# Performance work log

Measured on AMD Instinct MI355X. Metric: run time of the kernel, lower is better.

## Reference

```python
import jax, jax.numpy as jnp
import numpy as np

N = 100000        # nodes
E = 600000        # edges
D = 128           # entity_dim = hidden_dim = output_dim
H = 8             # heads
C = D // H        # per-head channels (TransformerConv out_channels)
L = 3             # num_layers
NUM_ENT = 500000
NUM_REL = 1000


def setup_inputs() -> dict:
    key = jax.random.key(0)
    ks = jax.random.split(key, 12)
    s = 0.02
    node_ids = jax.random.randint(ks[0], (N,), 0, NUM_ENT)
    edge_index = jax.random.randint(ks[1], (2, E), 0, N)
    edge_type = jax.random.randint(ks[2], (E,), 0, NUM_REL)
    # embeddings with padding_idx=0 zeroed (matches nn.Embedding(padding_idx=0))
    ent_emb = (jax.random.normal(ks[3], (NUM_ENT, D), jnp.float32) * s).at[0].set(0.0)
    rel_emb = (jax.random.normal(ks[4], (NUM_REL, D), jnp.float32) * s).at[0].set(0.0)
    # TransformerConv linear layers (stacked over L layers, all 128->128)
    Wq = jax.random.normal(ks[5], (L, D, D), jnp.float32) * s
    Wk = jax.random.normal(ks[6], (L, D, D), jnp.float32) * s
    Wv = jax.random.normal(ks[7], (L, D, D), jnp.float32) * s
    We = jax.random.normal(ks[8], (L, D, D), jnp.float32) * s   # lin_edge
    Ws = jax.random.normal(ks[9], (L, D, D), jnp.float32) * s   # lin_skip (root_weight)
    bq = jnp.zeros((L, D), jnp.float32)
    bk = jnp.zeros((L, D), jnp.float32)
    bv = jnp.zeros((L, D), jnp.float32)
    be = jnp.zeros((L, D), jnp.float32)
    bs = jnp.zeros((L, D), jnp.float32)
    ln_g = jnp.ones((L, D), jnp.float32)
    ln_b = jnp.zeros((L, D), jnp.float32)
    return dict(node_ids=node_ids, edge_index=edge_index, edge_type=edge_type,
                ent_emb=ent_emb, rel_emb=rel_emb,
                Wq=Wq, bq=bq, Wk=Wk, bk=bk, Wv=Wv, bv=bv,
                We=We, be=be, Ws=Ws, bs=bs, ln_g=ln_g, ln_b=ln_b)


def _layer_norm(x, g, b, eps=1e-5):
    mu = x.mean(-1, keepdims=True)
    var = ((x - mu) ** 2).mean(-1, keepdims=True)
    return (x - mu) * jax.lax.rsqrt(var + eps) * g + b


def _transformer_conv(x, src, dst, eattr, Wq, bq, Wk, bk, Wv, bv, We, be, Ws, bs):
    # PyG TransformerConv, concat=True, root_weight=True, beta=False, eval mode.
    q = (x @ Wq + bq).reshape(N, H, C)
    k = (x @ Wk + bk).reshape(N, H, C)
    v = (x @ Wv + bv).reshape(N, H, C)
    e = (eattr @ We + be).reshape(E, H, C)
    k_e = k[src] + e                                  # [E,H,C]
    alpha = jnp.einsum('ehc,ehc->eh', q[dst], k_e) / jnp.sqrt(jnp.float32(C))
    # segment softmax over incoming edges of each destination node
    amax = jax.ops.segment_max(alpha, dst, num_segments=N)   # [N,H]
    ex = jnp.exp(alpha - amax[dst])
    denom = jax.ops.segment_sum(ex, dst, num_segments=N)     # [N,H]
    alpha = ex / (denom[dst] + 1e-16)
    msg = (v[src] + e) * alpha[..., None]             # [E,H,C]
    out = jax.ops.segment_sum(msg.reshape(E, H * C), dst, num_segments=N)
    return out + x @ Ws + bs                          # skip (root weight)


def reference(node_ids, edge_index, edge_type, ent_emb, rel_emb,
              Wq, bq, Wk, bk, Wv, bv, We, be, Ws, bs, ln_g, ln_b):
    x = ent_emb[node_ids]            # [N,D]
    eattr = rel_emb[edge_type]       # [E,D]
    src, dst = edge_index[0], edge_index[1]
    for i in range(L):
        x_new = _transformer_conv(x, src, dst, eattr,
                                  Wq[i], bq[i], Wk[i], bk[i], Wv[i], bv[i],
                                  We[i], be[i], Ws[i], bs[i])
        x_new = jax.nn.relu(_layer_norm(x_new, ln_g[i], ln_b[i]))
        x = x + x_new                # dims match every layer -> residual
    graph_embedding = x.mean(axis=0, keepdims=True)
    return x, graph_embedding
```

## Files before the change

kernel.cpp:

```cpp
#include <hip/hip_runtime.h>

#define NN 100000
#define EE 600000
#define RR 1000

typedef unsigned short u16;
typedef __attribute__((ext_vector_type(8))) short short8;
typedef __attribute__((ext_vector_type(4))) float f32x4;

__device__ __forceinline__ float bf2f(u16 u) {
    union { unsigned int i; float f; } c; c.i = ((unsigned int)u) << 16; return c.f;
}
__device__ __forceinline__ u16 f2bf(float f) {
    union { float f; unsigned int i; } c; c.f = f;
    unsigned int x = c.i;
    return (u16)((x + 0x7FFFu + ((x >> 16) & 1u)) >> 16);
}
__device__ __forceinline__ unsigned int pack2bf(float a, float b) {
    return (unsigned int)f2bf(a) | ((unsigned int)f2bf(b) << 16);
}
__device__ __forceinline__ float ldin(const void* p, long long i, int f32) {
    if (f32) return ((const float*)p)[i];
    return bf2f(((const u16*)p)[i]);
}
__device__ __forceinline__ void stout(void* p, long long i, float v, int f32) {
    if (f32) ((float*)p)[i] = v;
    else     ((u16*)p)[i] = f2bf(v);
}

__global__ void GraphTransformerEncoder_35021163331783_kernel(
    int mode, int layer,
    const int* node_ids, const int* edge_index, const int* edge_type,
    const void* ent, const void* rel,
    const void* Wq, const void* bq, const void* Wk, const void* bk,
    const void* Wv, const void* bv, const void* We, const void* be,
    const void* Ws, const void* bs, const void* lng, const void* lnb,
    void* out,
    float* accum, float* erel, float* denom, float* gsum, float* flagp,
    u16* xb, u16* kb, u16* vb, u16* qb, u16* wbf)
{
    __shared__ float red[128];
    __shared__ __align__(16) u16 xt[32 * 128];
    __shared__ int scnt;
    int tid = blockIdx.x * blockDim.x + threadIdx.x;

    if (mode == 9) {
        if (threadIdx.x == 0) scnt = 0;
        __syncthreads();
        int bad = 0;
        for (int i = threadIdx.x; i < 8192; i += 256) {
            float v = bf2f(((const u16*)ent)[i]);
            if (!(fabsf(v) <= 1000.0f)) bad++;
        }
        atomicAdd(&scnt, bad);
        __syncthreads();
        if (threadIdx.x == 0) flagp[0] = (scnt > 64) ? 1.0f : 0.0f;
    } else if (mode == 0) {
        if (tid < 128) gsum[tid] = 0.0f;
        if (tid < NN * 128) {
            int isf32 = (flagp[0] != 0.0f);
            int n = tid >> 7, c = tid & 127;
            xb[tid] = f2bf(ldin(ent, (long long)node_ids[n] * 128 + c, isf32));
        }
    } else if (mode == 10) {
        if (tid < NN) ((int*)denom)[NN + tid] = 0;
    } else if (mode == 11) {
        if (tid < EE) {
            int dst = edge_index[EE + tid];
            atomicAdd(&((int*)denom)[NN + dst], 1);
        }
    } else if (mode == 12) {
        int* offs = (int*)denom;
        int* cnt  = offs + NN;
        int* wsum = (int*)red;
        int lane = threadIdx.x & 63, wid = threadIdx.x >> 6;
        int base = 0;
        for (int chunk = 0; chunk < NN; chunk += 1024) {
            int i = chunk + (int)threadIdx.x;
            int v = (i < NN) ? cnt[i] : 0;
            int incl = v;
            #pragma unroll
            for (int s = 1; s < 64; s <<= 1) {
                int t = __shfl_up(incl, s, 64);
                if (lane >= s) incl += t;
            }
            if (lane == 63) wsum[wid] = incl;
            __syncthreads();
            if (threadIdx.x == 0) {
                int run = 0;
                for (int w = 0; w < 16; ++w) { int t = wsum[w]; wsum[w] = run; run += t; }
                wsum[16] = run;
            }
            __syncthreads();
            int excl = base + wsum[wid] + incl - v;
            if (i < NN) { offs[i] = excl; cnt[i] = excl; }
            base += wsum[16];
            __syncthreads();
        }
    } else if (mode == 13) {
        if (tid < EE) {
            int src = edge_index[tid];
            int dst = edge_index[EE + tid];
            int rl  = edge_type[tid];
            int* cur = (int*)denom + NN;
            int pos = atomicAdd(&cur[dst], 1);
            ((unsigned int*)denom)[2 * NN + pos] =
                (unsigned int)src | ((unsigned int)rl << 17);
        }
    } else if (mode == 1) {
        if (tid < RR * 128) {
            int isf32 = (flagp[0] != 0.0f);
            int r = tid >> 7, d = tid & 127;
            float acc = 0.0f;
            for (int k = 0; k < 128; ++k)
                acc += ldin(rel, r * 128 + k, isf32)
                     * ldin(We, (long long)layer * 16384 + k * 128 + d, isf32);
            erel[tid] = acc + ldin(be, layer * 128 + d, isf32);
        }
    } else if (mode == 14) {
        if (tid < 4 * 16384) {
            int isf32 = (flagp[0] != 0.0f);
            int mat = tid >> 14;
            int rem = tid & 16383;
            int nt = rem >> 11;
            int ks = (rem >> 9) & 3;
            int l  = (rem >> 3) & 63;
            int j  = rem & 7;
            int k = ks * 32 + ((l >> 4) << 3) + j;
            int d = nt * 16 + (l & 15);
            const void* W = (mat == 0) ? Wq : (mat == 1) ? Wk : (mat == 2) ? Wv : Ws;
            wbf[tid] = f2bf(ldin(W, (long long)layer * 16384 + k * 128 + d, isf32));
        }
    } else if (mode == 2) {
        int n0 = blockIdx.x * 32;
        int t = threadIdx.x;
        for (int u = t; u < 512; u += 256) {
            int row = u >> 4, un = u & 15;
            uint4 d4 = *(const uint4*)(xb + (long long)(n0 + row) * 128 + un * 8);
            *(uint4*)(xt + row * 128 + ((un ^ (row & 7)) << 3)) = d4;
        }
        __syncthreads();
        int wv = t >> 6;
        int l  = t & 63;
        int lr = l & 15, lg = l >> 4;
        const u16* wf = wbf + (long long)wv * 16384;
        f32x4 acc[2][8];
        #pragma unroll
        for (int mt = 0; mt < 2; ++mt)
            #pragma unroll
            for (int nt = 0; nt < 8; ++nt) acc[mt][nt] = (f32x4)0.0f;
        #pragma unroll
        for (int ks = 0; ks < 4; ++ks) {
            int un = ks * 4 + lg;
            int r0 = lr, r1 = 16 + lr;
            short8 a0 = *(const short8*)(xt + r0 * 128 + ((un ^ (r0 & 7)) << 3));
            short8 a1 = *(const short8*)(xt + r1 * 128 + ((un ^ (r1 & 7)) << 3));
            short8 b[8];
            #pragma unroll
            for (int nt = 0; nt < 8; ++nt)
                b[nt] = *(const short8*)(wf + (((nt * 4 + ks) * 64 + l) << 3));
            #pragma unroll
            for (int nt = 0; nt < 8; ++nt) {
                acc[0][nt] = __builtin_amdgcn_mfma_f32_16x16x32_bf16(a0, b[nt], acc[0][nt], 0, 0, 0);
                acc[1][nt] = __builtin_amdgcn_mfma_f32_16x16x32_bf16(a1, b[nt], acc[1][nt], 0, 0, 0);
            }
        }
        int isf32 = (flagp[0] != 0.0f);
        const void* bias = (wv == 0) ? bq : (wv == 1) ? bk : (wv == 2) ? bv : bs;
        #pragma unroll
        for (int nt = 0; nt < 8; ++nt) {
            int col = nt * 16 + lr;
            float bc = ldin(bias, layer * 128 + col, isf32);
            #pragma unroll
            for (int mt = 0; mt < 2; ++mt) {
                #pragma unroll
                for (int v = 0; v < 4; ++v) {
                    int row = n0 + mt * 16 + lg * 4 + v;
                    long long o = (long long)row * 128 + col;
                    float val = acc[mt][nt][v] + bc;
                    if (wv == 0) qb[o] = f2bf(val);
                    else if (wv == 1) kb[o] = f2bf(val);
                    else if (wv == 2) vb[o] = f2bf(val);
                    else accum[o] = val;
                }
            }
        }
    } else if (mode == 4) {
        long long n = (long long)blockIdx.x * 4 + (threadIdx.x >> 6);
        if (n < NN) {
            int l = threadIdx.x & 63;
            int isf32 = (flagp[0] != 0.0f);
            const int* offs = (const int*)denom;
            const unsigned int* packed = (const unsigned int*)denom + 2 * NN;
            unsigned int qu = ((const unsigned int*)(qb + n * 128))[l];
            float q0 = bf2f((u16)(qu & 0xFFFFu)), q1 = bf2f((u16)(qu >> 16));
            float2 seed = ((const float2*)(accum + n * 128))[l];
            int beg = offs[n];
            int end = (n == NN - 1) ? EE : offs[n + 1];
            float m0 = 0.0f, m1 = 0.0f, dsum = 0.0f;
            for (int base = beg; base < end; base += 4) {
                int cnt = end - base;
                unsigned int ku[4], vu[4];
                float2 ef[4];
                #pragma unroll
                for (int j = 0; j < 4; ++j) {
                    if (j < cnt) {
                        unsigned int pk = packed[base + j];
                        long long src = (long long)(pk & 0x1FFFFu);
                        int rl = (int)(pk >> 17);
                        ku[j] = ((const unsigned int*)(kb + src * 128))[l];
                        vu[j] = ((const unsigned int*)(vb + src * 128))[l];
                        ef[j] = ((const float2*)(erel + rl * 128))[l];
                    }
                }
                #pragma unroll
                for (int j = 0; j < 4; ++j) {
                    if (j < cnt) {
                        float e0 = ef[j].x, e1 = ef[j].y;
                        float t = q0 * (bf2f((u16)(ku[j] & 0xFFFFu)) + e0)
                                + q1 * (bf2f((u16)(ku[j] >> 16)) + e1);
                        t += __shfl_xor(t, 1, 8);
                        t += __shfl_xor(t, 2, 8);
                        t += __shfl_xor(t, 4, 8);
                        float w = __expf(t * 0.25f);
                        dsum += w;
                        m0 += w * (bf2f((u16)(vu[j] & 0xFFFFu)) + e0);
                        m1 += w * (bf2f((u16)(vu[j] >> 16)) + e1);
                    }
                }
            }
            float inv = 1.0f / (dsum + 1e-16f);
            float o0 = seed.x + m0 * inv;
            float o1 = seed.y + m1 * inv;
            float s = o0 + o1;
            #pragma unroll
            for (int m = 1; m < 64; m <<= 1) s += __shfl_xor(s, m, 64);
            float mean = s * 0.0078125f;
            float d0 = o0 - mean, d1 = o1 - mean;
            float vs = d0 * d0 + d1 * d1;
            #pragma unroll
            for (int m = 1; m < 64; m <<= 1) vs += __shfl_xor(vs, m, 64);
            float rs = rsqrtf(vs * 0.0078125f + 1e-5f);
            float y0 = d0 * rs * ldin(lng, layer * 128 + 2 * l, isf32)
                     + ldin(lnb, layer * 128 + 2 * l, isf32);
            float y1 = d1 * rs * ldin(lng, layer * 128 + 2 * l + 1, isf32)
                     + ldin(lnb, layer * 128 + 2 * l + 1, isf32);
            if (y0 < 0.0f) y0 = 0.0f;
            if (y1 < 0.0f) y1 = 0.0f;
            unsigned int xu = ((const unsigned int*)(xb + n * 128))[l];
            float xv0 = bf2f((u16)(xu & 0xFFFFu)) + y0;
            float xv1 = bf2f((u16)(xu >> 16)) + y1;
            ((unsigned int*)(xb + n * 128))[l] = pack2bf(xv0, xv1);
            ((float2*)(accum + n * 128))[l] = make_float2(xv0, xv1);
        }
    } else if (mode == 5) {
        if (tid < NN * 128) {
            int isf32 = (flagp[0] != 0.0f);
            stout(out, tid, accum[tid], isf32);
        }
    } else if (mode == 7) {
        int c = threadIdx.x;
        float acc = 0.0f;
        for (long long n = blockIdx.x; n < NN; n += gridDim.x)
            acc += accum[n * 128 + c];
        atomicAdd(&gsum[c], acc);
    } else if (mode == 8) {
        if (tid < 128) {
            int isf32 = (flagp[0] != 0.0f);
            stout(out, (long long)NN * 128 + tid, gsum[tid] * (1.0f / (float)NN), isf32);
        }
    }
}

#define GTE_ARGS node_ids, edge_index, edge_type, ent, rel, Wq, bq, Wk, bk, \
    Wv, bv, We, be, Ws, bs, lng, lnb, out, accum, erel, denom, gsum, flagp, \
    xb, kb, vb, qb, wbf

extern "C" void kernel_launch(void* const* d_in, const int* in_sizes, int n_in,
                              void* d_out, int out_size, void* d_ws, size_t ws_size,
                              hipStream_t stream) {
    (void)in_sizes; (void)n_in; (void)out_size; (void)ws_size;

    const int* node_ids   = (const int*)d_in[0];
    const int* edge_index = (const int*)d_in[1];
    const int* edge_type  = (const int*)d_in[2];
    const void* ent = d_in[3];
    const void* rel = d_in[4];
    const void* Wq  = d_in[5];
    const void* bq  = d_in[6];
    const void* Wk  = d_in[7];
    const void* bk  = d_in[8];
    const void* Wv  = d_in[9];
    const void* bv  = d_in[10];
    const void* We  = d_in[11];
    const void* be  = d_in[12];
    const void* Ws  = d_in[13];
    const void* bs  = d_in[14];
    const void* lng = d_in[15];
    const void* lnb = d_in[16];
    void* out = d_out;

    float* accum = (float*)d_ws;
    float* erel  = accum + 12800000;
    float* denom = erel  + 128000;
    float* gsum  = denom + 800000;
    float* flagp = gsum  + 128;
    u16* xb = (u16*)(flagp + 64);
    u16* kb = xb + 12800000;
    u16* vb = kb + 12800000;
    u16* wbf = vb + 12800000;
    u16* qb = (u16*)d_out;

    GraphTransformerEncoder_35021163331783_kernel<<<1, 256, 0, stream>>>(9, 0, GTE_ARGS);
    GraphTransformerEncoder_35021163331783_kernel<<<50000, 256, 0, stream>>>(0, 0, GTE_ARGS);
    GraphTransformerEncoder_35021163331783_kernel<<<391, 256, 0, stream>>>(10, 0, GTE_ARGS);
    GraphTransformerEncoder_35021163331783_kernel<<<2344, 256, 0, stream>>>(11, 0, GTE_ARGS);
    GraphTransformerEncoder_35021163331783_kernel<<<1, 1024, 0, stream>>>(12, 0, GTE_ARGS);
    GraphTransformerEncoder_35021163331783_kernel<<<2344, 256, 0, stream>>>(13, 0, GTE_ARGS);
    for (int l = 0; l < 3; ++l) {
        GraphTransformerEncoder_35021163331783_kernel<<<500, 256, 0, stream>>>(1, l, GTE_ARGS);
        GraphTransformerEncoder_35021163331783_kernel<<<256, 256, 0, stream>>>(14, l, GTE_ARGS);
        GraphTransformerEncoder_35021163331783_kernel<<<3125, 256, 0, stream>>>(2, l, GTE_ARGS);
        GraphTransformerEncoder_35021163331783_kernel<<<25000, 256, 0, stream>>>(4, l, GTE_ARGS);
    }
    GraphTransformerEncoder_35021163331783_kernel<<<50000, 256, 0, stream>>>(5, 0, GTE_ARGS);
    GraphTransformerEncoder_35021163331783_kernel<<<512, 128, 0, stream>>>(7, 0, GTE_ARGS);
    GraphTransformerEncoder_35021163331783_kernel<<<1, 128, 0, stream>>>(8, 0, GTE_ARGS);
}
```

Baseline: 1.389 ms.

## Interleave K/V rows, widen edge unroll, and fuse final output with mean reduction

K and V projections are now stored interleaved in one buffer, so each edge gather in the attention/aggregation pass does a single 8-byte load per lane instead of two 4-byte loads from separate rows. The edge loop is unrolled to 8 edges to keep more gathers in flight. The fp32 residual copy is written only on the last layer. The final output store and the column-sum for the graph mean are fused into one kernel, removing a full pass over the fp32 activations. The trade-offs are more live registers per thread and a doubled-width K/V buffer layout.

```diff
diff --git a/kernel.cpp b/kernel.cpp
--- a/kernel.cpp
+++ b/kernel.cpp
@@ -37,7 +37,7 @@
     const void* Ws, const void* bs, const void* lng, const void* lnb,
     void* out,
     float* accum, float* erel, float* denom, float* gsum, float* flagp,
-    u16* xb, u16* kb, u16* vb, u16* qb, u16* wbf)
+    u16* xb, u16* kvb, u16* qb, u16* wbf)
 {
     __shared__ float red[128];
     __shared__ __align__(16) u16 xt[32 * 128];
@@ -179,8 +179,10 @@
                     long long o = (long long)row * 128 + col;
                     float val = acc[mt][nt][v] + bc;
                     if (wv == 0) qb[o] = f2bf(val);
-                    else if (wv == 1) kb[o] = f2bf(val);
-                    else if (wv == 2) vb[o] = f2bf(val);
+                    else if (wv == 1)
+                        kvb[(long long)row * 256 + ((col >> 1) << 2) + (col & 1)] = f2bf(val);
+                    else if (wv == 2)
+                        kvb[(long long)row * 256 + ((col >> 1) << 2) + 2 + (col & 1)] = f2bf(val);
                     else accum[o] = val;
                 }
             }
@@ -198,34 +200,33 @@
             int beg = offs[n];
             int end = (n == NN - 1) ? EE : offs[n + 1];
             float m0 = 0.0f, m1 = 0.0f, dsum = 0.0f;
-            for (int base = beg; base < end; base += 4) {
+            for (int base = beg; base < end; base += 8) {
                 int cnt = end - base;
-                unsigned int ku[4], vu[4];
-                float2 ef[4];
+                uint2 kv[8];
+                float2 ef[8];
                 #pragma unroll
-                for (int j = 0; j < 4; ++j) {
+                for (int j = 0; j < 8; ++j) {
                     if (j < cnt) {
                         unsigned int pk = packed[base + j];
                         long long src = (long long)(pk & 0x1FFFFu);
                         int rl = (int)(pk >> 17);
-                        ku[j] = ((const unsigned int*)(kb + src * 128))[l];
-                        vu[j] = ((const unsigned int*)(vb + src * 128))[l];
+                        kv[j] = ((const uint2*)(kvb + src * 256))[l];
                         ef[j] = ((const float2*)(erel + rl * 128))[l];
                     }
                 }
                 #pragma unroll
-                for (int j = 0; j < 4; ++j) {
+                for (int j = 0; j < 8; ++j) {
                     if (j < cnt) {
                         float e0 = ef[j].x, e1 = ef[j].y;
-                        float t = q0 * (bf2f((u16)(ku[j] & 0xFFFFu)) + e0)
-                                + q1 * (bf2f((u16)(ku[j] >> 16)) + e1);
+                        float t = q0 * (bf2f((u16)(kv[j].x & 0xFFFFu)) + e0)
+                                + q1 * (bf2f((u16)(kv[j].x >> 16)) + e1);
                         t += __shfl_xor(t, 1, 8);
                         t += __shfl_xor(t, 2, 8);
                         t += __shfl_xor(t, 4, 8);
                         float w = __expf(t * 0.25f);
                         dsum += w;
-                        m0 += w * (bf2f((u16)(vu[j] & 0xFFFFu)) + e0);
-                        m1 += w * (bf2f((u16)(vu[j] >> 16)) + e1);
+                        m0 += w * (bf2f((u16)(kv[j].y & 0xFFFFu)) + e0);
+                        m1 += w * (bf2f((u16)(kv[j].y >> 16)) + e1);
                     }
                 }
             }
@@ -251,19 +252,23 @@
             float xv0 = bf2f((u16)(xu & 0xFFFFu)) + y0;
             float xv1 = bf2f((u16)(xu >> 16)) + y1;
             ((unsigned int*)(xb + n * 128))[l] = pack2bf(xv0, xv1);
-            ((float2*)(accum + n * 128))[l] = make_float2(xv0, xv1);
+            if (layer == 2)
+                ((float2*)(accum + n * 128))[l] = make_float2(xv0, xv1);
         }
     } else if (mode == 5) {
-        if (tid < NN * 128) {
-            int isf32 = (flagp[0] != 0.0f);
-            stout(out, tid, accum[tid], isf32);
-        }
-    } else if (mode == 7) {
-        int c = threadIdx.x;
+        int c = threadIdx.x & 127;
+        int half = threadIdx.x >> 7;
+        int isf32 = (flagp[0] != 0.0f);
         float acc = 0.0f;
-        for (long long n = blockIdx.x; n < NN; n += gridDim.x)
-            acc += accum[n * 128 + c];
-        atomicAdd(&gsum[c], acc);
+        for (long long n = (long long)blockIdx.x * 2 + half; n < NN;
+             n += (long long)gridDim.x * 2) {
+            float v = accum[n * 128 + c];
+            stout(out, n * 128 + c, v, isf32);
+            acc += v;
+        }
+        if (half) red[c] = acc;
+        __syncthreads();
+        if (!half) atomicAdd(&gsum[c], acc + red[c]);
     } else if (mode == 8) {
         if (tid < 128) {
             int isf32 = (flagp[0] != 0.0f);
@@ -274,7 +279,7 @@
 
 #define GTE_ARGS node_ids, edge_index, edge_type, ent, rel, Wq, bq, Wk, bk, \
     Wv, bv, We, be, Ws, bs, lng, lnb, out, accum, erel, denom, gsum, flagp, \
-    xb, kb, vb, qb, wbf
+    xb, kvb, qb, wbf
 
 extern "C" void kernel_launch(void* const* d_in, const int* in_sizes, int n_in,
                               void* d_out, int out_size, void* d_ws, size_t ws_size,
@@ -305,11 +310,10 @@
     float* denom = erel  + 128000;
     float* gsum  = denom + 800000;
     float* flagp = gsum  + 128;
-    u16* xb = (u16*)(flagp + 64);
-    u16* kb = xb + 12800000;
-    u16* vb = kb + 12800000;
-    u16* wbf = vb + 12800000;
-    u16* qb = (u16*)d_out;
+    u16* xb  = (u16*)(flagp + 64);
+    u16* kvb = xb + 12800000;
+    u16* wbf = kvb + 25600000;
+    u16* qb  = (u16*)d_out;
 
     GraphTransformerEncoder_35021163331783_kernel<<<1, 256, 0, stream>>>(9, 0, GTE_ARGS);
     GraphTransformerEncoder_35021163331783_kernel<<<50000, 256, 0, stream>>>(0, 0, GTE_ARGS);
@@ -323,7 +327,6 @@
         GraphTransformerEncoder_35021163331783_kernel<<<3125, 256, 0, stream>>>(2, l, GTE_ARGS);
         GraphTransformerEncoder_35021163331783_kernel<<<25000, 256, 0, stream>>>(4, l, GTE_ARGS);
     }
-    GraphTransformerEncoder_35021163331783_kernel<<<50000, 256, 0, stream>>>(5, 0, GTE_ARGS);
-    GraphTransformerEncoder_35021163331783_kernel<<<512, 128, 0, stream>>>(7, 0, GTE_ARGS);
+    GraphTransformerEncoder_35021163331783_kernel<<<512, 256, 0, stream>>>(5, 0, GTE_ARGS);
     GraphTransformerEncoder_35021163331783_kernel<<<1, 128, 0, stream>>>(8, 0, GTE_ARGS);
 }
```

Result: faster. 1.336 ms (-3.8%).
